# Kernel tuning notes

Measured on AMD Instinct MI355X. Metric: run time of the kernel, lower is better.

The kernel has to match this reference:

```python
import jax, jax.numpy as jnp
import numpy as np

HEAD_DIM = 64


def setup_inputs() -> dict:
    key = jax.random.key(0)
    ks = jax.random.split(key, 7)
    B, T, S = 8, 256, 4096
    E, KV = 512, 768          # embed_dim, kv_dim
    H, D = 8, HEAD_DIM        # num_heads, head_dim
    x = jax.random.normal(ks[0], (B, T, E), dtype=jnp.float32)
    context = jax.random.normal(ks[1], (B, S, KV), dtype=jnp.float32)
    key_padding_mask = jax.random.randint(ks[2], (B, S), 0, 2) > 0  # True = ignore
    Wq = jax.random.normal(ks[3], (H * D, E), dtype=jnp.float32) * 0.02
    Wkv = jax.random.normal(ks[4], (2 * H * D, KV), dtype=jnp.float32) * 0.02
    Wo = jax.random.normal(ks[5], (E, H * D), dtype=jnp.float32) * 0.02
    bo = jnp.zeros((E,), dtype=jnp.float32)
    return {"x": x, "context": context, "key_padding_mask": key_padding_mask,
            "Wq": Wq, "Wkv": Wkv, "Wo": Wo, "bo": bo}


def reference(x, context, key_padding_mask, Wq, Wkv, Wo, bo):
    B, T, _ = x.shape
    S = context.shape[1]
    D = HEAD_DIM
    H = Wq.shape[0] // D
    scale = D ** (-0.5)

    # q: (B, H, T, D)
    q = (x @ Wq.T).reshape(B, T, H, D).transpose(0, 2, 1, 3)
    # kv: (B, S, 2, H, D) -> k, v each (B, H, S, D)
    kv = (context @ Wkv.T).reshape(B, S, 2, H, D)
    k = kv[:, :, 0].transpose(0, 2, 1, 3)
    v = kv[:, :, 1].transpose(0, 2, 1, 3)

    # attention scores (B, H, T, S) -- materialized, matching att_weights capture
    attn = jnp.einsum('bhtd,bhsd->bhts', q, k) * scale
    attn = jnp.where(key_padding_mask[:, None, None, :], -jnp.inf, attn)
    attn = jax.nn.softmax(attn, axis=-1)  # dropout p=0.0 -> identity

    out = jnp.einsum('bhts,bhsd->bthd', attn, v).reshape(B, T, H * D)
    return out @ Wo.T + bo
```

## Files before the change

kernel.cpp:

```cpp
#include <hip/hip_runtime.h>
#include <hip/hip_bf16.h>


typedef float f32x4 __attribute__((ext_vector_type(4)));
typedef __bf16 bf16x8 __attribute__((ext_vector_type(8)));
typedef unsigned short u16x8 __attribute__((ext_vector_type(8)));
typedef unsigned short u16x4 __attribute__((ext_vector_type(4)));
typedef unsigned int u32x4 __attribute__((ext_vector_type(4)));

static __device__ __forceinline__ unsigned short f2bf(float f) {
  return __builtin_bit_cast(unsigned short, (__bf16)f);
}
static __device__ __forceinline__ unsigned pk2(float lo, float hi) {
  return (unsigned)f2bf(lo) | ((unsigned)f2bf(hi) << 16);
}
static __device__ __forceinline__ f32x4 mfma16(bf16x8 a, bf16x8 b, f32x4 c) {
  return __builtin_amdgcn_mfma_f32_16x16x32_bf16(a, b, c, 0, 0, 0);
}
static __device__ __forceinline__ bf16x8 ld_frag(const unsigned short* lds, int byteOff) {
  return __builtin_bit_cast(bf16x8, *(const u16x8*)((const char*)lds + byteOff));
}
static __device__ __forceinline__ void gll16(const void* g, void* l) {
  __builtin_amdgcn_global_load_lds((__attribute__((address_space(1))) void*)(void*)g,
                                   (__attribute__((address_space(3))) void*)l, 16, 0, 0);
}
static __device__ __forceinline__ int swz4(int row) {
  return (row + (row >> 1)) & 3;
}

template <int OUTMODE, typename TA>
__global__ __launch_bounds__(256) void gemm_bt(
    const TA* __restrict__ A, const float* __restrict__ Bw,
    int M, int N, int K,
    unsigned short* __restrict__ o16a, unsigned short* __restrict__ o16b,
    float* __restrict__ oF, const float* __restrict__ bias) {
  __shared__ unsigned short As[2][128 * 32];
  __shared__ unsigned short Bs[2][128 * 32];
  const int tid = threadIdx.x;
  const int l = tid & 63, wid = tid >> 6;
  const int wr = wid >> 1, wc = wid & 1;
  const int r = l & 15, g = l >> 4;

  long m0, n0;
  if constexpr (OUTMODE == 1) {
    int bid = blockIdx.x;
    int xcd = bid & 7, j = bid >> 3;
    m0 = (long)(xcd * 32 + (j >> 3)) * 128;
    n0 = (long)(j & 7) * 128;
  } else {
    m0 = (long)blockIdx.y * 128;
    n0 = (long)blockIdx.x * 128;
  }

  const int srow = tid >> 1, sseg = tid & 1;
  const int sz = swz4(srow);
  const int wb0 = srow * 64 + (((sseg * 2) ^ sz) << 4);
  const int wb1 = srow * 64 + (((sseg * 2 + 1) ^ sz) << 4);

  const TA* aptr = A + (m0 + srow) * (long)K + sseg * 16;
  const float* bptr = Bw + (n0 + srow) * (long)K + sseg * 16;

  f32x4 rA[4]; u16x8 rAh[2]; f32x4 rB[4];
  auto loadT = [&](int kt) {
    if constexpr (sizeof(TA) == 4) {
      const f32x4* p = (const f32x4*)(aptr + kt * 32);
      rA[0] = p[0]; rA[1] = p[1]; rA[2] = p[2]; rA[3] = p[3];
    } else {
      const u16x8* p = (const u16x8*)(aptr + kt * 32);
      rAh[0] = p[0]; rAh[1] = p[1];
    }
    const f32x4* q = (const f32x4*)(bptr + kt * 32);
    rB[0] = q[0]; rB[1] = q[1]; rB[2] = q[2]; rB[3] = q[3];
  };
  auto writeT = [&](int sbuf) {
    char* ab = (char*)As[sbuf];
    if constexpr (sizeof(TA) == 4) {
      u32x4 lo = { pk2(rA[0][0], rA[0][1]), pk2(rA[0][2], rA[0][3]),
                   pk2(rA[1][0], rA[1][1]), pk2(rA[1][2], rA[1][3]) };
      u32x4 hi = { pk2(rA[2][0], rA[2][1]), pk2(rA[2][2], rA[2][3]),
                   pk2(rA[3][0], rA[3][1]), pk2(rA[3][2], rA[3][3]) };
      *(u32x4*)(ab + wb0) = lo; *(u32x4*)(ab + wb1) = hi;
    } else {
      *(u16x8*)(ab + wb0) = rAh[0]; *(u16x8*)(ab + wb1) = rAh[1];
    }
    char* bb = (char*)Bs[sbuf];
    u32x4 lo = { pk2(rB[0][0], rB[0][1]), pk2(rB[0][2], rB[0][3]),
                 pk2(rB[1][0], rB[1][1]), pk2(rB[1][2], rB[1][3]) };
    u32x4 hi = { pk2(rB[2][0], rB[2][1]), pk2(rB[2][2], rB[2][3]),
                 pk2(rB[3][0], rB[3][1]), pk2(rB[3][2], rB[3][3]) };
    *(u32x4*)(bb + wb0) = lo; *(u32x4*)(bb + wb1) = hi;
  };

  f32x4 acc[4][4] = {};
  const int nt = K >> 5;
  loadT(0); writeT(0);
  __syncthreads();
  int buf = 0;
  for (int t = 0; t < nt; ++t) {
    if (t + 1 < nt) loadT(t + 1);
    bf16x8 af[4], bfr[4];
#pragma unroll
    for (int m = 0; m < 4; ++m) {
      int row = wr * 64 + m * 16 + r;
      af[m] = ld_frag(As[buf], row * 64 + ((g ^ swz4(row)) << 4));
    }
#pragma unroll
    for (int n = 0; n < 4; ++n) {
      int row = wc * 64 + n * 16 + r;
      bfr[n] = ld_frag(Bs[buf], row * 64 + ((g ^ swz4(row)) << 4));
    }
#pragma unroll
    for (int m = 0; m < 4; ++m)
#pragma unroll
      for (int n = 0; n < 4; ++n)
        acc[m][n] = mfma16(af[m], bfr[n], acc[m][n]);
    if (t + 1 < nt) writeT(buf ^ 1);
    __syncthreads();
    buf ^= 1;
  }

#pragma unroll
  for (int m = 0; m < 4; ++m) {
#pragma unroll
    for (int n = 0; n < 4; ++n) {
      f32x4 v = acc[m][n];
      const long rg0 = m0 + wr * 64 + m * 16 + g * 4;
      const long cg = n0 + wc * 64 + n * 16 + r;
      if constexpr (OUTMODE == 0) {
#pragma unroll
        for (int i = 0; i < 4; ++i) {
          long rg = rg0 + i;
          int bb = (int)(rg >> 8), tt = (int)(rg & 255);
          int hh = (int)(cg >> 6), dd = (int)(cg & 63);
          o16a[(((long)(bb * 8 + hh) * 256 + tt) << 6) + dd] = f2bf(v[i]);
        }
      } else if constexpr (OUTMODE == 1) {
        if (cg < 512) {
          int hh = (int)(cg >> 6), dd = (int)(cg & 63);
#pragma unroll
          for (int i = 0; i < 4; ++i) {
            long rg = rg0 + i;
            int bb = (int)(rg >> 12), ss = (int)(rg & 4095);
            o16a[(((long)(bb * 8 + hh) * 4096 + ss) << 6) + dd] = f2bf(v[i]);
          }
        } else {
          int c2 = (int)(cg - 512);
          int hh = c2 >> 6, dd = c2 & 63;
          int bb = (int)(rg0 >> 12), ss = (int)(rg0 & 4095);
          u16x4 pk = { f2bf(v[0]), f2bf(v[1]), f2bf(v[2]), f2bf(v[3]) };
          *(u16x4*)&o16b[(((long)(bb * 8 + hh) * 64 + dd) << 12) + ss] = pk;
        }
      } else {
#pragma unroll
        for (int i = 0; i < 4; ++i) {
          long rg = rg0 + i;
          oF[rg * (long)N + cg] = v[i] + bias[cg];
        }
      }
    }
  }
}

__global__ __launch_bounds__(256) void attn_fwd(
    const unsigned short* __restrict__ qbuf,
    const unsigned short* __restrict__ kbuf,
    const unsigned short* __restrict__ vbuf,
    const int* __restrict__ mask,
    float* __restrict__ po, float* __restrict__ ml) {
  __shared__ unsigned short Ks[2][64 * 64];
  __shared__ unsigned short Vs[2][64 * 64];
  __shared__ unsigned short Ps[4][16 * 64];
  const int tid = threadIdx.x;
  const int l = tid & 63, w = tid >> 6;
  const int r = l & 15, g = l >> 4;
  const int bid = blockIdx.x;
  const int j = (bid & 7) * 128 + (bid >> 3);
  const int qt = j & 3, bh = (j >> 2) & 63, sp = j >> 8;

  const unsigned short* qrow = qbuf + (((long)bh * 256) + qt * 64 + w * 16 + r) * 64;
  const bf16x8 qf0 = __builtin_bit_cast(bf16x8, *(const u16x8*)(qrow + g * 8));
  const bf16x8 qf1 = __builtin_bit_cast(bf16x8, *(const u16x8*)(qrow + 32 + g * 8));

  f32x4 accO[4] = {};
  float mrow[4] = { -1e30f, -1e30f, -1e30f, -1e30f };
  float lrow[4] = {};
  const float SCL = 0.125f * 1.44269504088896340736f;

  const int s_base = sp * 1024;
  const unsigned short* kbase = kbuf + ((long)bh * 4096 + s_base) * 64;
  const unsigned short* vbase = vbuf + ((long)bh * 64) * 4096 + s_base;
  const int* mbase = mask + (bh >> 3) * 4096 + s_base;

  const int st_row = tid >> 3, st_c = tid & 7;
  auto stage = [&](int sbuf, int t0) {
#pragma unroll
    for (int p = 0; p < 2; ++p) {
      int row = p * 32 + st_row;
      int colb = (st_c * 16) ^ ((row & 7) << 4);
      int ldsOff = (p * 256 + tid) * 16;
      gll16(kbase + (long)(t0 + row) * 64 + (colb >> 1), (char*)Ks[sbuf] + ldsOff);
      gll16(vbase + (long)row * 4096 + t0 + (colb >> 1), (char*)Vs[sbuf] + ldsOff);
    }
  };

  stage(0, 0);
  asm volatile("s_waitcnt vmcnt(0)" ::: "memory");
  __builtin_amdgcn_s_barrier();
  __builtin_amdgcn_sched_barrier(0);

  int buf = 0;
  for (int it = 0; it < 16; ++it) {
    if (it + 1 < 16) stage(buf ^ 1, (it + 1) * 64);

    f32x4 sc[4] = {};
    __builtin_amdgcn_s_setprio(1);
#pragma unroll
    for (int nf = 0; nf < 4; ++nf) {
      int row = nf * 16 + r;
      int swz = (row & 7) << 4;
      bf16x8 k0 = ld_frag(Ks[buf], row * 128 + ((g * 16) ^ swz));
      bf16x8 k1 = ld_frag(Ks[buf], row * 128 + ((g * 16 + 64) ^ swz));
      sc[nf] = mfma16(qf0, k0, sc[nf]);
      sc[nf] = mfma16(qf1, k1, sc[nf]);
    }
    __builtin_amdgcn_s_setprio(0);

    float s[4][4];
#pragma unroll
    for (int nf = 0; nf < 4; ++nf) {
      bool mk = mbase[it * 64 + nf * 16 + r] != 0;
#pragma unroll
      for (int i = 0; i < 4; ++i) s[nf][i] = mk ? -1e30f : sc[nf][i] * SCL;
    }

    float tm[4], pr[4][4], rs[4], corr[4];
#pragma unroll
    for (int i = 0; i < 4; ++i) {
      tm[i] = fmaxf(fmaxf(s[0][i], s[1][i]), fmaxf(s[2][i], s[3][i]));
#pragma unroll
      for (int off = 1; off < 16; off <<= 1)
        tm[i] = fmaxf(tm[i], __shfl_xor(tm[i], off));
      float mn = fmaxf(mrow[i], tm[i]);
      corr[i] = exp2f(mrow[i] - mn);
      mrow[i] = mn;
      rs[i] = 0.f;
    }
#pragma unroll
    for (int nf = 0; nf < 4; ++nf)
#pragma unroll
      for (int i = 0; i < 4; ++i) {
        pr[nf][i] = exp2f(s[nf][i] - mrow[i]);
        rs[i] += pr[nf][i];
      }
#pragma unroll
    for (int i = 0; i < 4; ++i) {
#pragma unroll
      for (int off = 1; off < 16; off <<= 1)
        rs[i] += __shfl_xor(rs[i], off);
      lrow[i] = lrow[i] * corr[i] + rs[i];
    }
    f32x4 cv = { corr[0], corr[1], corr[2], corr[3] };
#pragma unroll
    for (int nf = 0; nf < 4; ++nf) accO[nf] *= cv;

    unsigned short* Pw = Ps[w];
#pragma unroll
    for (int nf = 0; nf < 4; ++nf)
#pragma unroll
      for (int i = 0; i < 4; ++i) {
        int prow = g * 4 + i;
        int pb = prow * 128 + ((((nf * 16 + r) * 2)) ^ ((prow & 7) << 4));
        *(unsigned short*)((char*)Pw + pb) = f2bf(pr[nf][i]);
      }
    asm volatile("s_waitcnt lgkmcnt(0)" ::: "memory");
    bf16x8 pf0 = ld_frag(Pw, r * 128 + ((g * 16) ^ ((r & 7) << 4)));
    bf16x8 pf1 = ld_frag(Pw, r * 128 + ((g * 16 + 64) ^ ((r & 7) << 4)));

    __builtin_amdgcn_s_setprio(1);
#pragma unroll
    for (int nf = 0; nf < 4; ++nf) {
      int row = nf * 16 + r;
      int swz = (row & 7) << 4;
      bf16x8 v0 = ld_frag(Vs[buf], row * 128 + ((g * 16) ^ swz));
      bf16x8 v1 = ld_frag(Vs[buf], row * 128 + ((g * 16 + 64) ^ swz));
      accO[nf] = mfma16(pf0, v0, accO[nf]);
      accO[nf] = mfma16(pf1, v1, accO[nf]);
    }
    __builtin_amdgcn_s_setprio(0);

    asm volatile("s_waitcnt vmcnt(0)" ::: "memory");
    __builtin_amdgcn_s_barrier();
    __builtin_amdgcn_sched_barrier(0);
    buf ^= 1;
  }

  const long rowg = (long)bh * 256 + qt * 64 + w * 16 + g * 4;
#pragma unroll
  for (int nf = 0; nf < 4; ++nf)
#pragma unroll
    for (int i = 0; i < 4; ++i)
      po[((long)sp * 16384 + rowg + i) * 64 + nf * 16 + r] = accO[nf][i];
  if (r == 0) {
#pragma unroll
    for (int i = 0; i < 4; ++i) {
      ml[((long)sp * 16384 + rowg + i) * 2 + 0] = mrow[i];
      ml[((long)sp * 16384 + rowg + i) * 2 + 1] = lrow[i];
    }
  }
}

__global__ __launch_bounds__(256) void attn_merge(
    const float* __restrict__ po, const float* __restrict__ ml,
    unsigned short* __restrict__ obuf) {
  const int idx = blockIdx.x * 256 + threadIdx.x;
  const int row = idx >> 2, dc = (idx & 3) << 4;
  float ms[4], ls[4], mx = -1e30f;
#pragma unroll
  for (int sp = 0; sp < 4; ++sp) {
    ms[sp] = ml[((long)sp * 16384 + row) * 2 + 0];
    ls[sp] = ml[((long)sp * 16384 + row) * 2 + 1];
    mx = fmaxf(mx, ms[sp]);
  }
  float lsum = 0.f, wg[4];
#pragma unroll
  for (int sp = 0; sp < 4; ++sp) { wg[sp] = exp2f(ms[sp] - mx); lsum += wg[sp] * ls[sp]; }
  const float inv = 1.f / lsum;
  f32x4 o[4] = {};
#pragma unroll
  for (int sp = 0; sp < 4; ++sp) {
    const f32x4* p = (const f32x4*)(po + ((long)sp * 16384 + row) * 64 + dc);
#pragma unroll
    for (int c = 0; c < 4; ++c) o[c] += wg[sp] * p[c];
  }
  u16x8 o0, o1;
#pragma unroll
  for (int k = 0; k < 8; ++k) {
    o0[k] = f2bf(o[k >> 2][k & 3] * inv);
    o1[k] = f2bf(o[2 + (k >> 2)][k & 3] * inv);
  }
  const long off = (((long)((row >> 11) * 256 + (row & 255))) << 9) + ((row >> 8) & 7) * 64 + dc;
  *(u16x8*)&obuf[off] = o0;
  *(u16x8*)&obuf[off + 8] = o1;
}

extern "C" void kernel_launch(void* const* d_in, const int* in_sizes, int n_in,
                              void* d_out, int out_size, void* d_ws, size_t ws_size,
                              hipStream_t stream) {
  (void)in_sizes; (void)n_in; (void)out_size; (void)ws_size;
  const float* x    = (const float*)d_in[0];
  const float* ctx  = (const float*)d_in[1];
  const int*   mask = (const int*)d_in[2];
  const float* Wq   = (const float*)d_in[3];
  const float* Wkv  = (const float*)d_in[4];
  const float* Wo   = (const float*)d_in[5];
  const float* bo   = (const float*)d_in[6];
  float* out = (float*)d_out;

  char* ws = (char*)d_ws;
  unsigned short* qbuf = (unsigned short*)(ws);
  unsigned short* kbuf = (unsigned short*)(ws + (size_t)2 * 1024 * 1024);
  unsigned short* vbuf = (unsigned short*)(ws + (size_t)34 * 1024 * 1024);
  unsigned short* obuf = (unsigned short*)(ws + (size_t)66 * 1024 * 1024);
  float* po = (float*)(ws + (size_t)68 * 1024 * 1024);
  float* ml = (float*)(ws + (size_t)84 * 1024 * 1024);

  gemm_bt<0, float><<<dim3(4, 16), 256, 0, stream>>>(
      x, Wq, 2048, 512, 512, qbuf, nullptr, nullptr, nullptr);
  gemm_bt<1, float><<<dim3(2048), 256, 0, stream>>>(
      ctx, Wkv, 32768, 1024, 768, kbuf, vbuf, nullptr, nullptr);
  attn_fwd<<<dim3(1024), 256, 0, stream>>>(qbuf, kbuf, vbuf, mask, po, ml);
  attn_merge<<<dim3(256), 256, 0, stream>>>(po, ml, obuf);
  gemm_bt<2, unsigned short><<<dim3(4, 16), 256, 0, stream>>>(
      obuf, Wo, 2048, 512, 512, nullptr, nullptr, out, bo);
}
```

Baseline: 213.7 us.

## Pre-convert context and Wkv to bf16 and use async LDS-load KV GEMM

Adds a separate pass that converts the fp32 context and Wkv to bf16 in workspace. A new dedicated KV projection GEMM then stages tiles straight into LDS with global_load_lds, replacing the old path that loaded fp32 into registers and converted in the GEMM. The aim is to halve the bytes the GEMM reads and overlap its loads with MFMA work. In exchange it adds an extra full read and write of the 100MB context tensor. ctxb aliases qbuf's workspace, which is safe only because the Q GEMM is launched after the KV GEMM.

```diff
diff --git a/kernel.cpp b/kernel.cpp
--- a/kernel.cpp
+++ b/kernel.cpp
@@ -28,11 +28,104 @@
   return (row + (row >> 1)) & 3;
 }
 
+__global__ __launch_bounds__(256) void cvt_bf16(const float* __restrict__ in,
+                                                unsigned short* __restrict__ out, int n8) {
+  int i = blockIdx.x * 256 + threadIdx.x;
+  if (i >= n8) return;
+  const f32x4* p = (const f32x4*)(in + (long)i * 8);
+  f32x4 a = p[0], b = p[1];
+  u16x8 o = { f2bf(a[0]), f2bf(a[1]), f2bf(a[2]), f2bf(a[3]),
+              f2bf(b[0]), f2bf(b[1]), f2bf(b[2]), f2bf(b[3]) };
+  *(u16x8*)(out + (long)i * 8) = o;
+}
+
+__global__ __launch_bounds__(256) void gemm_kv(
+    const unsigned short* __restrict__ A, const unsigned short* __restrict__ Bw,
+    unsigned short* __restrict__ kbuf, unsigned short* __restrict__ vbuf) {
+  constexpr int K = 768;
+  constexpr int NT = K / 32;
+  __shared__ unsigned short As[2][128 * 32];
+  __shared__ unsigned short Bs[2][128 * 32];
+  const int tid = threadIdx.x;
+  const int l = tid & 63, wid = tid >> 6;
+  const int wr = wid >> 1, wc = wid & 1;
+  const int r = l & 15, g = l >> 4;
+  const int bid = blockIdx.x;
+  const int xcd = bid & 7, j = bid >> 3;
+  const long m0 = (long)(xcd * 32 + (j >> 3)) * 128;
+  const long n0 = (long)(j & 7) * 128;
+
+  const int row0 = tid >> 2, cs = tid & 3;
+  const int gk0 = (cs ^ swz4(row0)) * 8;
+  const unsigned short* aR = A + (m0 + row0) * K + gk0;
+  const unsigned short* bR = Bw + (n0 + row0) * K + gk0;
+
+  auto stage = [&](int sbuf, int kt) {
+    const unsigned short* ap = aR + kt * 32;
+    const unsigned short* bp = bR + kt * 32;
+    gll16(ap,          (char*)As[sbuf] + tid * 16);
+    gll16(ap + 64 * K, (char*)As[sbuf] + 4096 + tid * 16);
+    gll16(bp,          (char*)Bs[sbuf] + tid * 16);
+    gll16(bp + 64 * K, (char*)Bs[sbuf] + 4096 + tid * 16);
+  };
+
+  f32x4 acc[4][4] = {};
+  stage(0, 0);
+  __syncthreads();
+  int buf = 0;
+  for (int t = 0; t < NT; ++t) {
+    if (t + 1 < NT) stage(buf ^ 1, t + 1);
+    bf16x8 af[4], bfr[4];
+#pragma unroll
+    for (int m = 0; m < 4; ++m) {
+      int row = wr * 64 + m * 16 + r;
+      af[m] = ld_frag(As[buf], row * 64 + ((g ^ swz4(row)) << 4));
+    }
+#pragma unroll
+    for (int n = 0; n < 4; ++n) {
+      int row = wc * 64 + n * 16 + r;
+      bfr[n] = ld_frag(Bs[buf], row * 64 + ((g ^ swz4(row)) << 4));
+    }
+#pragma unroll
+    for (int m = 0; m < 4; ++m)
+#pragma unroll
+      for (int n = 0; n < 4; ++n)
+        acc[m][n] = mfma16(af[m], bfr[n], acc[m][n]);
+    __syncthreads();
+    buf ^= 1;
+  }
+
+#pragma unroll
+  for (int m = 0; m < 4; ++m) {
+#pragma unroll
+    for (int n = 0; n < 4; ++n) {
+      f32x4 v = acc[m][n];
+      const long rg0 = m0 + wr * 64 + m * 16 + g * 4;
+      const long cg = n0 + wc * 64 + n * 16 + r;
+      if (cg < 512) {
+        int hh = (int)(cg >> 6), dd = (int)(cg & 63);
+#pragma unroll
+        for (int i = 0; i < 4; ++i) {
+          long rg = rg0 + i;
+          int bb = (int)(rg >> 12), ss = (int)(rg & 4095);
+          kbuf[(((long)(bb * 8 + hh) * 4096 + ss) << 6) + dd] = f2bf(v[i]);
+        }
+      } else {
+        int c2 = (int)(cg - 512);
+        int hh = c2 >> 6, dd = c2 & 63;
+        int bb = (int)(rg0 >> 12), ss = (int)(rg0 & 4095);
+        u16x4 pk = { f2bf(v[0]), f2bf(v[1]), f2bf(v[2]), f2bf(v[3]) };
+        *(u16x4*)&vbuf[(((long)(bb * 8 + hh) * 64 + dd) << 12) + ss] = pk;
+      }
+    }
+  }
+}
+
 template <int OUTMODE, typename TA>
 __global__ __launch_bounds__(256) void gemm_bt(
     const TA* __restrict__ A, const float* __restrict__ Bw,
     int M, int N, int K,
-    unsigned short* __restrict__ o16a, unsigned short* __restrict__ o16b,
+    unsigned short* __restrict__ o16a,
     float* __restrict__ oF, const float* __restrict__ bias) {
   __shared__ unsigned short As[2][128 * 32];
   __shared__ unsigned short Bs[2][128 * 32];
@@ -40,17 +133,7 @@
   const int l = tid & 63, wid = tid >> 6;
   const int wr = wid >> 1, wc = wid & 1;
   const int r = l & 15, g = l >> 4;
-
-  long m0, n0;
-  if constexpr (OUTMODE == 1) {
-    int bid = blockIdx.x;
-    int xcd = bid & 7, j = bid >> 3;
-    m0 = (long)(xcd * 32 + (j >> 3)) * 128;
-    n0 = (long)(j & 7) * 128;
-  } else {
-    m0 = (long)blockIdx.y * 128;
-    n0 = (long)blockIdx.x * 128;
-  }
+  const long m0 = (long)blockIdx.y * 128, n0 = (long)blockIdx.x * 128;
 
   const int srow = tid >> 1, sseg = tid & 1;
   const int sz = swz4(srow);
@@ -133,22 +216,6 @@
           int bb = (int)(rg >> 8), tt = (int)(rg & 255);
           int hh = (int)(cg >> 6), dd = (int)(cg & 63);
           o16a[(((long)(bb * 8 + hh) * 256 + tt) << 6) + dd] = f2bf(v[i]);
-        }
-      } else if constexpr (OUTMODE == 1) {
-        if (cg < 512) {
-          int hh = (int)(cg >> 6), dd = (int)(cg & 63);
-#pragma unroll
-          for (int i = 0; i < 4; ++i) {
-            long rg = rg0 + i;
-            int bb = (int)(rg >> 12), ss = (int)(rg & 4095);
-            o16a[(((long)(bb * 8 + hh) * 4096 + ss) << 6) + dd] = f2bf(v[i]);
-          }
-        } else {
-          int c2 = (int)(cg - 512);
-          int hh = c2 >> 6, dd = c2 & 63;
-          int bb = (int)(rg0 >> 12), ss = (int)(rg0 & 4095);
-          u16x4 pk = { f2bf(v[0]), f2bf(v[1]), f2bf(v[2]), f2bf(v[3]) };
-          *(u16x4*)&o16b[(((long)(bb * 8 + hh) * 64 + dd) << 12) + ss] = pk;
         }
       } else {
 #pragma unroll
@@ -357,19 +424,23 @@
   float* out = (float*)d_out;
 
   char* ws = (char*)d_ws;
-  unsigned short* qbuf = (unsigned short*)(ws);
-  unsigned short* kbuf = (unsigned short*)(ws + (size_t)2 * 1024 * 1024);
-  unsigned short* vbuf = (unsigned short*)(ws + (size_t)34 * 1024 * 1024);
-  unsigned short* obuf = (unsigned short*)(ws + (size_t)66 * 1024 * 1024);
-  float* po = (float*)(ws + (size_t)68 * 1024 * 1024);
-  float* ml = (float*)(ws + (size_t)84 * 1024 * 1024);
-
+  const size_t MiB = 1024 * 1024;
+  unsigned short* kbuf = (unsigned short*)(ws);
+  unsigned short* vbuf = (unsigned short*)(ws + 32 * MiB);
+  unsigned short* ctxb = (unsigned short*)(ws + 64 * MiB);
+  unsigned short* qbuf = (unsigned short*)(ws + 64 * MiB);
+  unsigned short* obuf = (unsigned short*)(ws + 66 * MiB);
+  float* po = (float*)(ws + 68 * MiB);
+  float* ml = (float*)(ws + 84 * MiB);
+  unsigned short* wkvb = (unsigned short*)(ws + 112 * MiB);
+
+  cvt_bf16<<<dim3(12288), 256, 0, stream>>>(ctx, ctxb, 3145728);
+  cvt_bf16<<<dim3(384), 256, 0, stream>>>(Wkv, wkvb, 98304);
+  gemm_kv<<<dim3(2048), 256, 0, stream>>>(ctxb, wkvb, kbuf, vbuf);
   gemm_bt<0, float><<<dim3(4, 16), 256, 0, stream>>>(
-      x, Wq, 2048, 512, 512, qbuf, nullptr, nullptr, nullptr);
-  gemm_bt<1, float><<<dim3(2048), 256, 0, stream>>>(
-      ctx, Wkv, 32768, 1024, 768, kbuf, vbuf, nullptr, nullptr);
+      x, Wq, 2048, 512, 512, qbuf, nullptr, nullptr);
   attn_fwd<<<dim3(1024), 256, 0, stream>>>(qbuf, kbuf, vbuf, mask, po, ml);
   attn_merge<<<dim3(256), 256, 0, stream>>>(po, ml, obuf);
   gemm_bt<2, unsigned short><<<dim3(4, 16), 256, 0, stream>>>(
-      obuf, Wo, 2048, 512, 512, nullptr, nullptr, out, bo);
-}
+      obuf, Wo, 2048, 512, 512, nullptr, out, bo);
+}
```

After: 198.9 us. 6.9% less time.
